# Performance work log

Hardware: AMD Instinct MI355X
Metric: run time of the kernel (lower is better)

## Reference

```python
import jax, jax.numpy as jnp
import numpy as np

EMBED_DIMS = [8, 16, 8]      # prod = 1024 = embed_dim
HIDDEN_DIMS = [16, 16, 16]   # prod = 4096 = hidden_dim
RANK = 16
B, S = 4, 1024


def _make_cores(key, in_dims, out_dims, rank):
    d = len(in_dims)
    ranks = [1] + [rank] * (d - 1) + [1]
    cores = []
    for k in range(d):
        key, sub = jax.random.split(key)
        shape = (ranks[k], in_dims[k], out_dims[k], ranks[k + 1])
        scale = 1.0 / np.sqrt(in_dims[k] * ranks[k])
        cores.append((scale * jax.random.normal(sub, shape, dtype=jnp.float32)))
    return cores


def setup_inputs() -> dict:
    key = jax.random.key(0)
    k_x, k1, k2, kb1, kb2 = jax.random.split(key, 5)
    x = jax.random.normal(k_x, (B, S, 1024), dtype=jnp.float32)
    fc1 = _make_cores(k1, EMBED_DIMS, HIDDEN_DIMS, RANK)
    fc2 = _make_cores(k2, HIDDEN_DIMS, EMBED_DIMS, RANK)
    b1 = 0.01 * jax.random.normal(kb1, (4096,), dtype=jnp.float32)
    b2 = 0.01 * jax.random.normal(kb2, (1024,), dtype=jnp.float32)
    return {
        "x": x,
        "fc1_c0": fc1[0], "fc1_c1": fc1[1], "fc1_c2": fc1[2], "fc1_b": b1,
        "fc2_c0": fc2[0], "fc2_c1": fc2[1], "fc2_c2": fc2[2], "fc2_b": b2,
    }


def tt_linear(x_flat, cores, bias, in_dims):
    """TT-matrix x batch-of-vectors product. x_flat: [N, prod(in_dims)].

    Cores: core_k has shape [r_{k-1}, n_k, m_k, r_k] with r_0 = r_d = 1.
    Invariant: acc is [r_{k-1}, n_k, rest] with rest laid out as
    (n_{k+1}..n_d, N, m_1..m_{k-1}).
    """
    N = x_flat.shape[0]
    acc = x_flat.reshape((N,) + tuple(in_dims))      # [N, n1..nd]
    acc = jnp.moveaxis(acc, 0, -1)                   # [n1..nd, N]
    acc = acc.reshape(in_dims[0], -1)[None]          # [1, n1, rest]
    d = len(cores)
    for k, c in enumerate(cores):
        # contract previous rank + current input mode
        acc = jnp.einsum('pnR,pnmq->Rmq', acc, c)    # [rest, m_k, r_k]
        if k < d - 1:
            n_next = in_dims[k + 1]
            R, m, q = acc.shape
            acc = acc.reshape(n_next, R // n_next, m, q)
            acc = jnp.transpose(acc, (3, 0, 1, 2)).reshape(q, n_next, -1)
    # final acc: [N * m1..m_{d-1}, m_d, 1] -> [N, M]
    return acc.reshape(N, -1) + bias


def reference(x, fc1_c0, fc1_c1, fc1_c2, fc1_b, fc2_c0, fc2_c1, fc2_c2, fc2_b):
    flat = x.reshape(-1, x.shape[-1])                        # [N, embed_dim]
    z1 = tt_linear(flat, [fc1_c0, fc1_c1, fc1_c2], fc1_b, EMBED_DIMS)   # [N, hidden]
    h1 = jax.nn.gelu(z1, approximate=False)                  # exact erf GELU (torch default)
    z2 = tt_linear(h1, [fc2_c0, fc2_c1, fc2_c2], fc2_b, HIDDEN_DIMS)    # [N, embed]
    return z2.reshape(*x.shape[:-1], z2.shape[-1])
```

## Files before the change

### kernel.cpp

```cpp
#include <hip/hip_runtime.h>
#include <stdint.h>

__device__ __forceinline__ float b2f(unsigned short u) {
    union { uint32_t i; float f; } v; v.i = ((uint32_t)u) << 16; return v.f;
}
__device__ __forceinline__ unsigned short f2b(float f) {
    union { float f; uint32_t i; } v; v.f = f;
    uint32_t r = v.i + 0x7fffu + ((v.i >> 16) & 1u);
    return (unsigned short)(r >> 16);
}

typedef __bf16 bf16x8 __attribute__((ext_vector_type(8)));
typedef float  f32x16 __attribute__((ext_vector_type(16)));

template<int N3, int M3>
__device__ __forceinline__ void build_T_body(int e,
                                             const float* __restrict__ c1,
                                             const float* __restrict__ c2,
                                             float* __restrict__ T) {
    int m3 = e % M3;
    int t  = e / M3;
    int n3 = t % N3;
    int rm = t / N3;
    float s = 0.f;
#pragma unroll
    for (int r2 = 0; r2 < 16; ++r2)
        s += c1[rm * 16 + r2] * c2[(r2 * N3 + n3) * M3 + m3];
    T[e] = s;
}

__global__ __launch_bounds__(256)
void prep_stage1(const float* __restrict__ c11, const float* __restrict__ c12,
                 float* __restrict__ T1,
                 const float* __restrict__ c21, const float* __restrict__ c22,
                 float* __restrict__ T2,
                 const float* __restrict__ x, unsigned short* __restrict__ xb) {
    const int b = blockIdx.x;
    if (b < 2048) {
        build_T_body<8, 16>(b * 256 + threadIdx.x, c11, c12, T1);
    } else if (b < 4096) {
        build_T_body<16, 8>((b - 2048) * 256 + threadIdx.x, c21, c22, T2);
    } else {
        const int t = (b - 4096) * 256 + threadIdx.x;
        const float4* p = (const float4*)(x + (size_t)t * 8);
        float4 f0 = p[0], f1 = p[1];
        int4 o;
        o.x = (uint32_t)f2b(f0.x) | ((uint32_t)f2b(f0.y) << 16);
        o.y = (uint32_t)f2b(f0.z) | ((uint32_t)f2b(f0.w) << 16);
        o.z = (uint32_t)f2b(f1.x) | ((uint32_t)f2b(f1.y) << 16);
        o.w = (uint32_t)f2b(f1.z) | ((uint32_t)f2b(f1.w) << 16);
        ((int4*)xb)[t] = o;
    }
}

template<int N1, int N2, int N3, int M1, int M2, int M3>
__device__ __forceinline__ void build_W_body(int t,
                                             const float* __restrict__ c0,
                                             const float* __restrict__ T,
                                             unsigned short* __restrict__ W) {
    constexpr int K = N1 * N2 * N3;
    int m3 = t % M3;
    int m2 = (t / M3) % M2;
    int n2 = (t / (M3 * M2)) % N2;
    int m1 = (t / (M3 * M2 * N2)) % M1;
    int n1 =  t / (M3 * M2 * N2 * M1);

    float c0r[16];
    const float4* c0p = (const float4*)(c0 + (n1 * M1 + m1) * 16);
#pragma unroll
    for (int i = 0; i < 4; ++i) ((float4*)c0r)[i] = c0p[i];

    float acc[N3] = {};
#pragma unroll
    for (int r1 = 0; r1 < 16; ++r1) {
        const float* Tp = T + (size_t)(((r1 * 16 + n2) * 16 + m2) * N3) * M3 + m3;
#pragma unroll
        for (int n3 = 0; n3 < N3; ++n3)
            acc[n3] += c0r[r1] * Tp[n3 * M3];
    }

    unsigned short ob[N3];
#pragma unroll
    for (int n3 = 0; n3 < N3; ++n3) ob[n3] = f2b(acc[n3]);

    unsigned short* dst = W + (size_t)((m1 * M2 + m2) * M3 + m3) * K
                            + (n1 * N2 + n2) * N3;
#pragma unroll
    for (int c = 0; c < N3 / 8; ++c)
        ((int4*)dst)[c] = ((const int4*)ob)[c];
}

__global__ __launch_bounds__(256)
void build_W_both(const float* __restrict__ c10, const float* __restrict__ T1,
                  unsigned short* __restrict__ W1,
                  const float* __restrict__ c20, const float* __restrict__ T2,
                  unsigned short* __restrict__ W2) {
    const int b = blockIdx.x;
    if (b < 2048)
        build_W_body<8, 16, 8, 16, 16, 16>(b * 256 + threadIdx.x, c10, T1, W1);
    else
        build_W_body<16, 16, 16, 8, 16, 8>((b - 2048) * 256 + threadIdx.x, c20, T2, W2);
}

template<int N1, int N2, int N3, int M1, int M2, int M3>
__global__ __launch_bounds__(256)
void build_W(const float* __restrict__ c0, const float* __restrict__ T,
             unsigned short* __restrict__ W) {
    build_W_body<N1, N2, N3, M1, M2, M3>(blockIdx.x * 256 + threadIdx.x, c0, T, W);
}

__global__ __launch_bounds__(256)
void bias_fill(const float* __restrict__ b, float4* __restrict__ out) {
    int t = blockIdx.x * 256 + threadIdx.x;
    out[t] = ((const float4*)b)[t & 255];
}

template<int BM, int BN, int KCH, int KSTR, int GX, int GY,
         bool DO_GELU, bool ATOMIC>
__global__ __launch_bounds__(256, 4)
void gemm_sb(const unsigned short* __restrict__ A,
             const unsigned short* __restrict__ Bt,
             const float* __restrict__ bias,
             void* __restrict__ Cv,
             int Ncols)
{
    constexpr int BK  = 64;
    constexpr int NT  = KCH / BK;
    constexpr int ASZ = BM * BK;
    constexpr int ACH = BM / 32;
    constexpr int BCH = BN / 32;
    constexpr int FI  = BM / 64, FJ = BN / 64;

    extern __shared__ unsigned short sh[];

    const int tid   = threadIdx.x;
    const int lane  = tid & 63;
    const int wave  = tid >> 6;
    const int m32   = lane & 31;
    const int khalf = lane >> 5;
    const int waveM = (wave >> 1) * (BM / 2);
    const int waveN = (wave & 1) * (BN / 2);
    const int srow  = tid >> 3;
    const int sslot = tid & 7;

    int lin = ((int)blockIdx.z * GY + (int)blockIdx.y) * GX + (int)blockIdx.x;
    const int total = GX * GY * (int)gridDim.z;
    lin = (lin & 7) * (total >> 3) + (lin >> 3);
    const int colBase = (lin % GX) * BN;
    const int rowBase = ((lin / GX) % GY) * BM;
    const int kOff    = (lin / (GX * GY)) * KCH;

#define SB_STAGE(K0_)                                                         \
    {                                                                         \
        _Pragma("unroll")                                                     \
        for (int c = 0; c < ACH; ++c) {                                       \
            const int r  = c * 32 + srow;                                     \
            const int jg = sslot ^ (r & 7) ^ ((r >> 3) & 7);                  \
            const unsigned short* src = A +                                   \
                (size_t)(rowBase + r) * KSTR + (K0_) + jg * 8;                \
            unsigned short* dst = sh + c * 2048 + wave * 512;                 \
            __builtin_amdgcn_global_load_lds(                                 \
                (const __attribute__((address_space(1))) void*)src,           \
                (__attribute__((address_space(3))) void*)dst, 16, 0, 0);      \
        }                                                                     \
        _Pragma("unroll")                                                     \
        for (int c = 0; c < BCH; ++c) {                                       \
            const int r  = c * 32 + srow;                                     \
            const int jg = sslot ^ (r & 7) ^ ((r >> 3) & 7);                  \
            const unsigned short* src = Bt +                                  \
                (size_t)(colBase + r) * KSTR + (K0_) + jg * 8;                \
            unsigned short* dst = sh + ASZ + c * 2048 + wave * 512;           \
            __builtin_amdgcn_global_load_lds(                                 \
                (const __attribute__((address_space(1))) void*)src,           \
                (__attribute__((address_space(3))) void*)dst, 16, 0, 0);      \
        }                                                                     \
    }

    f32x16 acc[FI][FJ] = {};

    for (int t = 0; t < NT; ++t) {
        SB_STAGE(kOff + t * BK)
        __syncthreads();

        const unsigned short* Ab = sh;
        const unsigned short* Bb = sh + ASZ;
#pragma unroll
        for (int ks = 0; ks < 4; ++ks) {
            bf16x8 a_f[FI], b_f[FJ];
            const int g = ks * 2 + khalf;
#pragma unroll
            for (int i = 0; i < FI; ++i) {
                const int r = waveM + i * 32 + m32;
                const int key = (r & 7) ^ ((r >> 3) & 7);
                a_f[i] = *(const bf16x8*)&Ab[r * BK + ((g ^ key) << 3)];
            }
#pragma unroll
            for (int j = 0; j < FJ; ++j) {
                const int r = waveN + j * 32 + m32;
                const int key = (r & 7) ^ ((r >> 3) & 7);
                b_f[j] = *(const bf16x8*)&Bb[r * BK + ((g ^ key) << 3)];
            }
#pragma unroll
            for (int i = 0; i < FI; ++i)
#pragma unroll
                for (int j = 0; j < FJ; ++j)
                    acc[i][j] = __builtin_amdgcn_mfma_f32_32x32x16_bf16(
                        a_f[i], b_f[j], acc[i][j], 0, 0, 0);
        }
        if (t + 1 < NT) __syncthreads();
    }
#undef SB_STAGE

#pragma unroll
    for (int i = 0; i < FI; ++i) {
#pragma unroll
        for (int j = 0; j < FJ; ++j) {
            const int col = colBase + waveN + j * 32 + m32;
            const float bv = ATOMIC ? 0.f : bias[col];
#pragma unroll
            for (int reg = 0; reg < 16; ++reg) {
                const int row = rowBase + waveM + i * 32 +
                                (reg & 3) + 8 * (reg >> 2) + 4 * khalf;
                const size_t off = (size_t)row * Ncols + col;
                if (ATOMIC) {
                    unsafeAtomicAdd((float*)Cv + off, acc[i][j][reg]);
                } else {
                    float z = acc[i][j][reg] + bv;
                    if (DO_GELU)
                        z = 0.5f * z * (1.f + erff(z * 0.70710678118654752f));
                    ((unsigned short*)Cv)[off] = f2b(z);
                }
            }
        }
    }
}

#define PC_COMPUTE(BUF)                                                       \
    {                                                                         \
        _Pragma("unroll")                                                     \
        for (int ks = 0; ks < 4; ++ks) {                                      \
            bf16x8 a_f[FI], b_f[FJ];                                          \
            _Pragma("unroll")                                                 \
            for (int i = 0; i < FI; ++i) {                                    \
                const int key = (m32 & 7) ^                                   \
                    (((waveM >> 3) + 4 * i + (m32 >> 3)) & 7);                \
                const int slot = ((ks * 2 + khalf) ^ key) * 8;                \
                a_f[i] = *(const bf16x8*)&As[(BUF) * ASZ +                    \
                          (waveM + i * 32 + m32) * BK + slot];                \
            }                                                                 \
            _Pragma("unroll")                                                 \
            for (int j = 0; j < FJ; ++j) {                                    \
                const int key = (m32 & 7) ^                                   \
                    (((waveN >> 3) + 4 * j + (m32 >> 3)) & 7);                \
                const int slot = ((ks * 2 + khalf) ^ key) * 8;                \
                b_f[j] = *(const bf16x8*)&Bs[(BUF) * BSZ +                    \
                          (waveN + j * 32 + m32) * BK + slot];                \
            }                                                                 \
            _Pragma("unroll")                                                 \
            for (int i = 0; i < FI; ++i)                                      \
                _Pragma("unroll")                                             \
                for (int j = 0; j < FJ; ++j)                                  \
                    acc[i][j] = __builtin_amdgcn_mfma_f32_32x32x16_bf16(      \
                        a_f[i], b_f[j], acc[i][j], 0, 0, 0);                  \
        }                                                                     \
    }

template<int BM, int BN, int KTOT, bool DO_GELU, bool A_F32, bool C_F32>
__global__ __launch_bounds__(512, 4)
void gemm_pc(const void* __restrict__ Av,
             const unsigned short* __restrict__ Bt,
             const float* __restrict__ bias,
             void* __restrict__ Cv,
             int Ncols) {
    constexpr int BK  = 64;
    constexpr int CA  = BM / 8;
    constexpr int CB  = BN / 8;
    constexpr int PA  = CA / 4;
    constexpr int PB  = CB / 4;
    constexpr int FI  = BM / 64;
    constexpr int FJ  = BN / 64;
    constexpr int ASZ = BM * BK;
    constexpr int BSZ = BN * BK;
    __shared__ unsigned short As[2 * ASZ];
    __shared__ unsigned short Bs[2 * BSZ];

    const int tid  = threadIdx.x;
    const int lane = tid & 63;
    const int wave = tid >> 6;
    const int rowBase = blockIdx.y * BM;
    const int colBase = blockIdx.x * BN;

    const int lr    = lane >> 3;
    const int jj    = lane & 7;
    const int m32   = lane & 31;
    const int khalf = lane >> 5;

    if (wave >= 4) {
        const int pw = wave - 4;
#pragma unroll
        for (int it = 0; it < PA; ++it) {
            const int c  = pw * PA + it;
            const int jg = jj ^ lr ^ (c & 7);
            const size_t aoff = (size_t)(rowBase + c * 8 + lr) * KTOT + jg * 8;
            int4 v;
            if (A_F32) {
                const float* ga = (const float*)Av + aoff;
                float4 f0 = *(const float4*)ga;
                float4 f1 = *(const float4*)(ga + 4);
                v.x = (uint32_t)f2b(f0.x) | ((uint32_t)f2b(f0.y) << 16);
                v.y = (uint32_t)f2b(f0.z) | ((uint32_t)f2b(f0.w) << 16);
                v.z = (uint32_t)f2b(f1.x) | ((uint32_t)f2b(f1.y) << 16);
                v.w = (uint32_t)f2b(f1.z) | ((uint32_t)f2b(f1.w) << 16);
            } else {
                v = *(const int4*)((const unsigned short*)Av + aoff);
            }
            *(int4*)&As[c * 512 + lane * 8] = v;
        }
#pragma unroll
        for (int it = 0; it < PB; ++it) {
            const int c  = pw * PB + it;
            const int jg = jj ^ lr ^ (c & 7);
            *(int4*)&Bs[c * 512 + lane * 8] =
                *(const int4*)(Bt + (size_t)(colBase + c * 8 + lr) * KTOT + jg * 8);
        }
        __syncthreads();

        int buf = 1;
        for (int k0 = BK; k0 < KTOT; k0 += BK) {
            int4 aR[PA], bR[PB];
#pragma unroll
            for (int it = 0; it < PA; ++it) {
                const int c  = pw * PA + it;
                const int jg = jj ^ lr ^ (c & 7);
                const size_t aoff = (size_t)(rowBase + c * 8 + lr) * KTOT + k0 + jg * 8;
                if (A_F32) {
                    const float* ga = (const float*)Av + aoff;
                    float4 f0 = *(const float4*)ga;
                    float4 f1 = *(const float4*)(ga + 4);
                    int4 v;
                    v.x = (uint32_t)f2b(f0.x) | ((uint32_t)f2b(f0.y) << 16);
                    v.y = (uint32_t)f2b(f0.z) | ((uint32_t)f2b(f0.w) << 16);
                    v.z = (uint32_t)f2b(f1.x) | ((uint32_t)f2b(f1.y) << 16);
                    v.w = (uint32_t)f2b(f1.z) | ((uint32_t)f2b(f1.w) << 16);
                    aR[it] = v;
                } else {
                    aR[it] = *(const int4*)((const unsigned short*)Av + aoff);
                }
            }
#pragma unroll
            for (int it = 0; it < PB; ++it) {
                const int c  = pw * PB + it;
                const int jg = jj ^ lr ^ (c & 7);
                bR[it] = *(const int4*)(Bt + (size_t)(colBase + c * 8 + lr) * KTOT + k0 + jg * 8);
            }
#pragma unroll
            for (int it = 0; it < PA; ++it) {
                const int c = pw * PA + it;
                *(int4*)&As[buf * ASZ + c * 512 + lane * 8] = aR[it];
            }
#pragma unroll
            for (int it = 0; it < PB; ++it) {
                const int c = pw * PB + it;
                *(int4*)&Bs[buf * BSZ + c * 512 + lane * 8] = bR[it];
            }
            __syncthreads();
            buf ^= 1;
        }
    } else {
        const int waveM = (wave >> 1) * (BM / 2);
        const int waveN = (wave & 1) * (BN / 2);
        f32x16 acc[FI][FJ] = {};

        __syncthreads();

        int cur = 0;
        for (int k0 = BK; k0 < KTOT; k0 += BK) {
            PC_COMPUTE(cur)
            __syncthreads();
            cur ^= 1;
        }
        PC_COMPUTE(cur)

#pragma unroll
        for (int i = 0; i < FI; ++i) {
#pragma unroll
            for (int j = 0; j < FJ; ++j) {
                const int col = colBase + waveN + j * 32 + m32;
                const float bv = bias[col];
#pragma unroll
                for (int reg = 0; reg < 16; ++reg) {
                    const int row = rowBase + waveM + i * 32 +
                                    (reg & 3) + 8 * (reg >> 2) + 4 * khalf;
                    float z = acc[i][j][reg] + bv;
                    if (DO_GELU)
                        z = 0.5f * z * (1.f + erff(z * 0.70710678118654752f));
                    const size_t off = (size_t)row * Ncols + col;
                    if (C_F32) ((float*)Cv)[off] = z;
                    else       ((unsigned short*)Cv)[off] = f2b(z);
                }
            }
        }
    }
}

extern "C" void kernel_launch(void* const* d_in, const int* in_sizes, int n_in,
                              void* d_out, int out_size, void* d_ws, size_t ws_size,
                              hipStream_t stream) {
    const float* x      = (const float*)d_in[0];
    const float* fc1_c0 = (const float*)d_in[1];
    const float* fc1_c1 = (const float*)d_in[2];
    const float* fc1_c2 = (const float*)d_in[3];
    const float* fc1_b  = (const float*)d_in[4];
    const float* fc2_c0 = (const float*)d_in[5];
    const float* fc2_c1 = (const float*)d_in[6];
    const float* fc2_c2 = (const float*)d_in[7];
    const float* fc2_b  = (const float*)d_in[8];

    float* T1 = (float*)d_out;
    float* T2 = (float*)d_out + 524288;
    unsigned short* xb = (unsigned short*)((char*)d_out + (4u << 20));

    char* ws = (char*)d_ws;
    const bool big = ws_size >= (48ull << 20);

    constexpr int DLDS = 40 << 10;

    prep_stage1<<<6144, 256, 0, stream>>>(fc1_c1, fc1_c2, T1,
                                          fc2_c1, fc2_c2, T2, x, xb);

    if (big) {
        unsigned short* W1 = (unsigned short*)ws;
        unsigned short* W2 = (unsigned short*)(ws + (8u << 20));
        unsigned short* h  = (unsigned short*)(ws + (16u << 20));

        build_W_both<<<3072, 256, 0, stream>>>(fc1_c0, T1, W1,
                                               fc2_c0, T2, W2);
        gemm_sb<128, 128, 1024, 1024, 32, 32, true, false>
            <<<dim3(32, 32, 1), 256, DLDS, stream>>>(xb, W1, fc1_b, h, 4096);
        bias_fill<<<4096, 256, 0, stream>>>(fc2_b, (float4*)d_out);
        gemm_sb<128, 64, 2048, 4096, 16, 32, false, true>
            <<<dim3(16, 32, 2), 256, DLDS, stream>>>(h, W2, fc2_b, d_out, 1024);
    } else {
        unsigned short* W = (unsigned short*)ws;
        unsigned short* h = (unsigned short*)(ws + (8u << 20));

        build_W<8, 16, 8, 16, 16, 16><<<2048, 256, 0, stream>>>(fc1_c0, T1, W);
        gemm_pc<128, 128, 1024, true, false, false>
            <<<dim3(32, 32), 512, 0, stream>>>(xb, W, fc1_b, h, 4096);
        build_W<16, 16, 16, 8, 16, 8><<<1024, 256, 0, stream>>>(fc2_c0, T2, W);
        gemm_pc<128, 64, 4096, false, false, true>
            <<<dim3(16, 32), 512, 0, stream>>>(h, W, fc2_b, d_out, 1024);
    }
}
```

Measured before the change: 235.7 us.

## Fuse TT weight construction and x cast into one prep kernel; drop split-K

```diff
diff --git a/kernel.cpp b/kernel.cpp
--- a/kernel.cpp
+++ b/kernel.cpp
@@ -12,6 +12,80 @@
 
 typedef __bf16 bf16x8 __attribute__((ext_vector_type(8)));
 typedef float  f32x16 __attribute__((ext_vector_type(16)));
+
+template<int N1, int N2, int N3, int M1, int M2, int M3>
+__device__ __forceinline__ void build_W_fused(int blk,
+                                              const float* __restrict__ c0,
+                                              const float* __restrict__ c1,
+                                              const float* __restrict__ c2,
+                                              unsigned short* __restrict__ W,
+                                              float* __restrict__ S) {
+    constexpr int K = N1 * N2 * N3;
+    const int n2 = blk / M2;
+    const int m2 = blk % M2;
+
+    for (int e = threadIdx.x; e < 16 * N3 * M3; e += 256) {
+        const int m3 = e % M3;
+        const int n3 = (e / M3) % N3;
+        const int r1 = e / (M3 * N3);
+        const float* c1p = c1 + ((r1 * N2 + n2) * M2 + m2) * 16;
+        float s = 0.f;
+#pragma unroll
+        for (int r2 = 0; r2 < 16; ++r2)
+            s += c1p[r2] * c2[(r2 * N3 + n3) * M3 + m3];
+        S[e] = s;
+    }
+    __syncthreads();
+
+    for (int e = threadIdx.x; e < N1 * M1 * M3; e += 256) {
+        const int m3 = e % M3;
+        const int m1 = (e / M3) % M1;
+        const int n1 = e / (M3 * M1);
+        const float* c0p = c0 + (n1 * M1 + m1) * 16;
+        float acc[N3] = {};
+#pragma unroll
+        for (int r1 = 0; r1 < 16; ++r1) {
+            const float c0v = c0p[r1];
+#pragma unroll
+            for (int n3 = 0; n3 < N3; ++n3)
+                acc[n3] += c0v * S[(r1 * N3 + n3) * M3 + m3];
+        }
+        unsigned short ob[N3];
+#pragma unroll
+        for (int n3 = 0; n3 < N3; ++n3) ob[n3] = f2b(acc[n3]);
+        unsigned short* dst = W + (size_t)((m1 * M2 + m2) * M3 + m3) * K
+                                + (n1 * N2 + n2) * N3;
+#pragma unroll
+        for (int c = 0; c < N3 / 8; ++c)
+            ((int4*)dst)[c] = ((const int4*)ob)[c];
+    }
+}
+
+__global__ __launch_bounds__(256)
+void prep_all(const float* __restrict__ c10, const float* __restrict__ c11,
+              const float* __restrict__ c12,
+              const float* __restrict__ c20, const float* __restrict__ c21,
+              const float* __restrict__ c22,
+              const float* __restrict__ x, unsigned short* __restrict__ xb,
+              unsigned short* __restrict__ W1, unsigned short* __restrict__ W2) {
+    __shared__ float S[16 * 128];
+    const int b = blockIdx.x;
+    if (b < 256) {
+        build_W_fused<8, 16, 8, 16, 16, 16>(b, c10, c11, c12, W1, S);
+    } else if (b < 512) {
+        build_W_fused<16, 16, 16, 8, 16, 8>(b - 256, c20, c21, c22, W2, S);
+    } else {
+        const int t = (b - 512) * 256 + threadIdx.x;
+        const float4* p = (const float4*)(x + (size_t)t * 8);
+        float4 f0 = p[0], f1 = p[1];
+        int4 o;
+        o.x = (uint32_t)f2b(f0.x) | ((uint32_t)f2b(f0.y) << 16);
+        o.y = (uint32_t)f2b(f0.z) | ((uint32_t)f2b(f0.w) << 16);
+        o.z = (uint32_t)f2b(f1.x) | ((uint32_t)f2b(f1.y) << 16);
+        o.w = (uint32_t)f2b(f1.z) | ((uint32_t)f2b(f1.w) << 16);
+        ((int4*)xb)[t] = o;
+    }
+}
 
 template<int N3, int M3>
 __device__ __forceinline__ void build_T_body(int e,
@@ -90,29 +164,11 @@
         ((int4*)dst)[c] = ((const int4*)ob)[c];
 }
 
-__global__ __launch_bounds__(256)
-void build_W_both(const float* __restrict__ c10, const float* __restrict__ T1,
-                  unsigned short* __restrict__ W1,
-                  const float* __restrict__ c20, const float* __restrict__ T2,
-                  unsigned short* __restrict__ W2) {
-    const int b = blockIdx.x;
-    if (b < 2048)
-        build_W_body<8, 16, 8, 16, 16, 16>(b * 256 + threadIdx.x, c10, T1, W1);
-    else
-        build_W_body<16, 16, 16, 8, 16, 8>((b - 2048) * 256 + threadIdx.x, c20, T2, W2);
-}
-
 template<int N1, int N2, int N3, int M1, int M2, int M3>
 __global__ __launch_bounds__(256)
 void build_W(const float* __restrict__ c0, const float* __restrict__ T,
              unsigned short* __restrict__ W) {
     build_W_body<N1, N2, N3, M1, M2, M3>(blockIdx.x * 256 + threadIdx.x, c0, T, W);
-}
-
-__global__ __launch_bounds__(256)
-void bias_fill(const float* __restrict__ b, float4* __restrict__ out) {
-    int t = blockIdx.x * 256 + threadIdx.x;
-    out[t] = ((const float4*)b)[t & 255];
 }
 
 template<int BM, int BN, int KCH, int KSTR, int GX, int GY,
@@ -228,7 +284,9 @@
                     float z = acc[i][j][reg] + bv;
                     if (DO_GELU)
                         z = 0.5f * z * (1.f + erff(z * 0.70710678118654752f));
-                    ((unsigned short*)Cv)[off] = f2b(z);
+                    if (ATOMIC) ((float*)Cv)[off] = z;
+                    else if (DO_GELU) ((unsigned short*)Cv)[off] = f2b(z);
+                    else ((float*)Cv)[off] = z;
                 }
             }
         }
@@ -416,34 +474,33 @@
     const float* fc2_c2 = (const float*)d_in[7];
     const float* fc2_b  = (const float*)d_in[8];
 
-    float* T1 = (float*)d_out;
-    float* T2 = (float*)d_out + 524288;
-    unsigned short* xb = (unsigned short*)((char*)d_out + (4u << 20));
-
     char* ws = (char*)d_ws;
     const bool big = ws_size >= (48ull << 20);
 
     constexpr int DLDS = 40 << 10;
 
-    prep_stage1<<<6144, 256, 0, stream>>>(fc1_c1, fc1_c2, T1,
-                                          fc2_c1, fc2_c2, T2, x, xb);
-
     if (big) {
+        unsigned short* xb = (unsigned short*)d_out;
         unsigned short* W1 = (unsigned short*)ws;
         unsigned short* W2 = (unsigned short*)(ws + (8u << 20));
         unsigned short* h  = (unsigned short*)(ws + (16u << 20));
 
-        build_W_both<<<3072, 256, 0, stream>>>(fc1_c0, T1, W1,
-                                               fc2_c0, T2, W2);
+        prep_all<<<2560, 256, 0, stream>>>(fc1_c0, fc1_c1, fc1_c2,
+                                           fc2_c0, fc2_c1, fc2_c2,
+                                           x, xb, W1, W2);
         gemm_sb<128, 128, 1024, 1024, 32, 32, true, false>
             <<<dim3(32, 32, 1), 256, DLDS, stream>>>(xb, W1, fc1_b, h, 4096);
-        bias_fill<<<4096, 256, 0, stream>>>(fc2_b, (float4*)d_out);
-        gemm_sb<128, 64, 2048, 4096, 16, 32, false, true>
-            <<<dim3(16, 32, 2), 256, DLDS, stream>>>(h, W2, fc2_b, d_out, 1024);
+        gemm_sb<128, 64, 4096, 4096, 16, 32, false, false>
+            <<<dim3(16, 32, 1), 256, DLDS, stream>>>(h, W2, fc2_b, d_out, 1024);
     } else {
+        float* T1 = (float*)d_out;
+        float* T2 = (float*)d_out + 524288;
+        unsigned short* xb = (unsigned short*)((char*)d_out + (4u << 20));
         unsigned short* W = (unsigned short*)ws;
         unsigned short* h = (unsigned short*)(ws + (8u << 20));
 
+        prep_stage1<<<6144, 256, 0, stream>>>(fc1_c1, fc1_c2, T1,
+                                              fc2_c1, fc2_c2, T2, x, xb);
         build_W<8, 16, 8, 16, 16, 16><<<2048, 256, 0, stream>>>(fc1_c0, T1, W);
         gemm_pc<128, 128, 1024, true, false, false>
             <<<dim3(32, 32), 512, 0, stream>>>(xb, W, fc1_b, h, 4096);
```

After: 211.7 us. 1.11x faster.
